# Performance work log

Hardware: AMD Instinct MI355X
Metric: run time of the kernel (lower is better)

The kernel has to match this reference:

```python
import jax, jax.numpy as jnp
import numpy as np


def _prelu(x, a):
    return jnp.where(x >= 0, x, a * x)


def _conv1x1(x, w, b, a):
    # x: (B,C,H,W), w: (O,C), b: (O,), a: PReLU scalar (shared, torch default)
    y = jnp.einsum('bchw,oc->bohw', x, w) + b[None, :, None, None]
    return _prelu(y, a)


def setup_inputs() -> dict:
    key = jax.random.key(0)
    ks = jax.random.split(key, 7)
    B, C, H, W = 8, 128, 256, 256
    std = 1.0 / np.sqrt(C)
    x = jax.random.normal(ks[0], (B, C, H, W), dtype=jnp.float32)
    Wf = jax.random.normal(ks[1], (C, C), dtype=jnp.float32) * std
    bf = jax.random.normal(ks[2], (C,), dtype=jnp.float32) * std
    Wg = jax.random.normal(ks[3], (C, C), dtype=jnp.float32) * std
    bg = jax.random.normal(ks[4], (C,), dtype=jnp.float32) * std
    Wh = jax.random.normal(ks[5], (C, C), dtype=jnp.float32) * std
    bh = jax.random.normal(ks[6], (C,), dtype=jnp.float32) * std
    af = jnp.float32(0.25)
    ag = jnp.float32(0.25)
    ah = jnp.float32(0.25)
    return {"x": x, "Wf": Wf, "bf": bf, "af": af,
            "Wg": Wg, "bg": bg, "ag": ag,
            "Wh": Wh, "bh": bh, "ah": ah}


def reference(x, Wf, bf, af, Wg, bg, ag, Wh, bh, ah):
    # 1x1 conv projections + PReLU
    map_f = _conv1x1(x, Wf, bf, af)          # (B,C,H,W)
    map_g = _conv1x1(x, Wg, bg, ag)          # (B,C,H,W)
    map_h = _conv1x1(x, Wh, bh, ah)          # (B,C,H,W)
    # map_f.transpose(2,3) @ map_g -> (B,C,W,W), unscaled single-head attention
    atten = jnp.einsum('bchw,bchv->bcwv', map_f, map_g)  # (B,C,W,W)
    atten = jax.nn.softmax(atten, axis=-1)
    # map_h @ atten -> (B,C,H,W)
    out = jnp.einsum('bchw,bcwv->bchv', map_h, atten)
    return out + x
```

## Files before the change

kernel.cpp:

```cpp
#include <hip/hip_runtime.h>

typedef __bf16 bf16_t;
typedef __bf16 bf16x8 __attribute__((ext_vector_type(8)));
typedef __bf16 bf16x4 __attribute__((ext_vector_type(4)));
typedef float  f32x4  __attribute__((ext_vector_type(4)));

#define HW_ 65536
#define C_  128

__device__ __forceinline__ int swz(int r) { return ((r ^ (r >> 3)) & 7) << 4; }

#define LGKM0()  asm volatile("s_waitcnt lgkmcnt(0)" ::: "memory")
#define VMCNT0() asm volatile("s_waitcnt vmcnt(0)" ::: "memory")
__device__ __forceinline__ void BAR() {
  asm volatile("" ::: "memory");
  __builtin_amdgcn_s_barrier();
  asm volatile("" ::: "memory");
}

typedef __attribute__((address_space(1))) const unsigned int g_u32;
typedef __attribute__((address_space(3))) unsigned int l_u32;

__global__ void wprep_kernel(const float* __restrict__ Wf, const float* __restrict__ Wg,
                             const float* __restrict__ Wh, bf16_t* __restrict__ dst)
{
  int i = blockIdx.x * 256 + threadIdx.x;
  int o = i >> 7, c = i & 127;
  int boff = (o * 256 + c * 2) ^ swz(o);
  char* d = (char*)dst;
  *(bf16_t*)(d + boff)         = (bf16_t)Wf[i];
  *(bf16_t*)(d + 32768 + boff) = (bf16_t)Wg[i];
  *(bf16_t*)(d + 65536 + boff) = (bf16_t)Wh[i];
}

__device__ __forceinline__ void stage_w(char* lds, const bf16_t* __restrict__ Wimg,
                                        int wv, int t)
{
  #pragma unroll
  for (int rep = 0; rep < 8; ++rep) {
    const char* src = (const char*)Wimg + (rep * 256 + t) * 16;
    char* dst = lds + 32768 + (rep * 4 + wv) * 1024;
    __builtin_amdgcn_global_load_lds((g_u32*)src, (l_u32*)dst, 16, 0, 0);
  }
}

__device__ __forceinline__ void conv_mfma(const char* lds, f32x4 (&acc)[2][8],
                                          int wv, int lr, int lq)
{
  const f32x4 fz = {0.f, 0.f, 0.f, 0.f};
  #pragma unroll
  for (int mf = 0; mf < 2; ++mf)
    #pragma unroll
    for (int nf = 0; nf < 8; ++nf)
      acc[mf][nf] = fz;

  #pragma unroll
  for (int ks = 0; ks < 4; ++ks) {
    int kb = ks * 32 + lq * 8;
    bf16x8 a[2], bb[8];
    #pragma unroll
    for (int mf = 0; mf < 2; ++mf) {
      int m = wv * 32 + mf * 16 + lr;
      a[mf] = *(const bf16x8*)(lds + 32768 + ((m * 256 + kb * 2) ^ swz(m)));
    }
    #pragma unroll
    for (int nf = 0; nf < 8; ++nf) {
      int n = nf * 16 + lr;
      bb[nf] = *(const bf16x8*)(lds + ((n * 256 + kb * 2) ^ swz(n)));
    }
    #pragma unroll
    for (int mf = 0; mf < 2; ++mf)
      #pragma unroll
      for (int nf = 0; nf < 8; ++nf)
        acc[mf][nf] = __builtin_amdgcn_mfma_f32_16x16x32_bf16(a[mf], bb[nf], acc[mf][nf], 0, 0, 0);
  }
}

template<bool HBLK>
__device__ __forceinline__ void conv_epi(const f32x4 (&acc)[2][8],
                                         const float* __restrict__ bias, float alpha,
                                         bf16_t* __restrict__ dst, size_t pb,
                                         int wv, int lr, int lq, int s0)
{
  #pragma unroll
  for (int mf = 0; mf < 2; ++mf) {
    #pragma unroll
    for (int i = 0; i < 4; ++i) {
      int o = wv * 32 + mf * 16 + lq * 4 + i;
      float bo = bias[o];
      #pragma unroll
      for (int nf = 0; nf < 8; ++nf) {
        int s = s0 + nf * 16 + lr;
        float v = acc[mf][nf][i] + bo;
        v = (v >= 0.f) ? v : alpha * v;
        size_t off;
        if (HBLK) {
          int h = s >> 8, w = s & 255;
          off = pb + (size_t)o * HW_ + (size_t)(w >> 6) * 16384 + h * 64 + (w & 63);
        } else {
          off = pb + (size_t)o * HW_ + s;
        }
        dst[off] = (bf16_t)v;
      }
    }
  }
}

__global__ __launch_bounds__(256, 2) void conv_kernel(
    const float* __restrict__ x, const bf16_t* __restrict__ Wimg,
    const float* __restrict__ bfp, const float* __restrict__ afp,
    const float* __restrict__ bgp, const float* __restrict__ agp,
    const float* __restrict__ bhp, const float* __restrict__ ahp,
    bf16_t* __restrict__ mF, bf16_t* __restrict__ mG, bf16_t* __restrict__ mH, int b0)
{
  __shared__ __align__(16) char lds[65536];
  const int t = threadIdx.x;
  const int bloc = blockIdx.y;
  const int s0 = blockIdx.x * 128;
  const size_t xbase = ((size_t)(b0 + bloc) * C_) * HW_ + s0;
  const int wv = t >> 6, lane = t & 63, lr = lane & 15, lq = lane >> 4;
  const size_t pb = (size_t)bloc * C_ * HW_;

  stage_w(lds, Wimg, wv, t);

  #pragma unroll
  for (int rep = 0; rep < 4; ++rep) {
    int q = rep * 256 + t;
    int c0 = (q >> 5) * 4, sl0 = (q & 31) * 4;
    f32x4 r[4];
    #pragma unroll
    for (int i = 0; i < 4; ++i)
      r[i] = *(const f32x4*)(x + xbase + (size_t)(c0 + i) * HW_ + sl0);
    #pragma unroll
    for (int js = 0; js < 4; ++js) {
      int s = sl0 + js;
      bf16x4 v;
      v[0] = (bf16_t)r[0][js]; v[1] = (bf16_t)r[1][js];
      v[2] = (bf16_t)r[2][js]; v[3] = (bf16_t)r[3][js];
      *(bf16x4*)(lds + ((s * 256 + c0 * 2) ^ swz(s))) = v;
    }
  }
  __syncthreads();

  f32x4 acc[2][8];

  conv_mfma(lds, acc, wv, lr, lq);
  BAR();
  stage_w(lds, Wimg + 16384, wv, t);
  conv_epi<false>(acc, bfp, afp[0], mF, pb, wv, lr, lq, s0);
  VMCNT0(); BAR();

  conv_mfma(lds, acc, wv, lr, lq);
  BAR();
  stage_w(lds, Wimg + 32768, wv, t);
  conv_epi<false>(acc, bgp, agp[0], mG, pb, wv, lr, lq, s0);
  VMCNT0(); BAR();

  conv_mfma(lds, acc, wv, lr, lq);
  conv_epi<true>(acc, bhp, ahp[0], mH, pb, wv, lr, lq, s0);
}

#define GT_OFF  32768
#define HS_OFF  131072
#define SMAX_OFF 151552
#define SSUM_OFF 153600
#define SMEM_BYTES 155648

__global__ __launch_bounds__(512, 2) void attn_kernel(
    const bf16_t* __restrict__ mF, const bf16_t* __restrict__ mG, const bf16_t* __restrict__ mH,
    const float* __restrict__ x, float* __restrict__ out, int b0)
{
  extern __shared__ __align__(16) char smem[];
  const int t = threadIdx.x;
  const int c = blockIdx.x, bloc = blockIdx.y;
  const int wv = t >> 6, lane = t & 63, lr = lane & 15, lq = lane >> 4;
  const int wr = wv >> 1, wc = wv & 1;
  const size_t plane  = ((size_t)bloc * C_ + c) * HW_;
  const size_t gplane = (((size_t)(b0 + bloc)) * C_ + c) * HW_;

  const f32x4 fz = {0.f, 0.f, 0.f, 0.f};
  f32x4 acc[4][8];
  #pragma unroll
  for (int mf = 0; mf < 4; ++mf)
    #pragma unroll
    for (int nf = 0; nf < 8; ++nf)
      acc[mf][nf] = fz;

  const int hq = t >> 5, wb8 = t & 31;

  bf16x8 pfF[4], pfG[4];
  #pragma unroll
  for (int i = 0; i < 4; ++i) {
    pfF[i] = *(const bf16x8*)(mF + plane + (size_t)(hq * 4 + i) * 256 + wb8 * 8);
    pfG[i] = *(const bf16x8*)(mG + plane + (size_t)(hq * 4 + i) * 256 + wb8 * 8);
  }

  for (int hb = 0; hb < 256; hb += 64) {
    BAR();
    #pragma unroll
    for (int j = 0; j < 8; ++j) {
      int w = wb8 * 8 + j;
      bf16x4 v; v[0] = pfF[0][j]; v[1] = pfF[1][j]; v[2] = pfF[2][j]; v[3] = pfF[3][j];
      *(bf16x4*)(smem + ((w * 128 + hq * 8) ^ swz(w))) = v;
      bf16x4 g; g[0] = pfG[0][j]; g[1] = pfG[1][j]; g[2] = pfG[2][j]; g[3] = pfG[3][j];
      *(bf16x4*)(smem + GT_OFF + ((w * 128 + hq * 8) ^ swz(w))) = g;
    }
    if (hb < 192) {
      #pragma unroll
      for (int i = 0; i < 4; ++i) {
        pfF[i] = *(const bf16x8*)(mF + plane + (size_t)(hb + 64 + hq * 4 + i) * 256 + wb8 * 8);
        pfG[i] = *(const bf16x8*)(mG + plane + (size_t)(hb + 64 + hq * 4 + i) * 256 + wb8 * 8);
      }
    }
    LGKM0(); BAR();
    #pragma unroll
    for (int k0 = 0; k0 < 64; k0 += 32) {
      int kb = k0 + lq * 8;
      bf16x8 a[4], bb[8];
      #pragma unroll
      for (int mf = 0; mf < 4; ++mf) {
        int m = wr * 64 + mf * 16 + lr;
        a[mf] = *(const bf16x8*)(smem + ((m * 128 + kb * 2) ^ swz(m)));
      }
      #pragma unroll
      for (int nf = 0; nf < 8; ++nf) {
        int n = wc * 128 + nf * 16 + lr;
        bb[nf] = *(const bf16x8*)(smem + GT_OFF + ((n * 128 + kb * 2) ^ swz(n)));
      }
      #pragma unroll
      for (int mf = 0; mf < 4; ++mf)
        #pragma unroll
        for (int nf = 0; nf < 8; ++nf)
          acc[mf][nf] = __builtin_amdgcn_mfma_f32_16x16x32_bf16(a[mf], bb[nf], acc[mf][nf], 0, 0, 0);
    }
  }

  float* smax = (float*)(smem + SMAX_OFF);
  float* ssum = (float*)(smem + SSUM_OFF);
  float rowm[4][4];
  #pragma unroll
  for (int mf = 0; mf < 4; ++mf)
    #pragma unroll
    for (int i = 0; i < 4; ++i) {
      float m = acc[mf][0][i];
      #pragma unroll
      for (int nf = 1; nf < 8; ++nf) m = fmaxf(m, acc[mf][nf][i]);
      #pragma unroll
      for (int d = 1; d < 16; d <<= 1) m = fmaxf(m, __shfl_xor(m, d));
      rowm[mf][i] = m;
    }
  if (lr == 0) {
    #pragma unroll
    for (int mf = 0; mf < 4; ++mf)
      #pragma unroll
      for (int i = 0; i < 4; ++i)
        smax[wc * 256 + wr * 64 + mf * 16 + lq * 4 + i] = rowm[mf][i];
  }
  __syncthreads();
  float m2[4][4], rs[4][4];
  #pragma unroll
  for (int mf = 0; mf < 4; ++mf)
    #pragma unroll
    for (int i = 0; i < 4; ++i) {
      int w = wr * 64 + mf * 16 + lq * 4 + i;
      m2[mf][i] = fmaxf(smax[w], smax[256 + w]);
      rs[mf][i] = 0.f;
    }
  #pragma unroll
  for (int mf = 0; mf < 4; ++mf)
    #pragma unroll
    for (int nf = 0; nf < 8; ++nf)
      #pragma unroll
      for (int i = 0; i < 4; ++i) {
        float e = __expf(acc[mf][nf][i] - m2[mf][i]);
        acc[mf][nf][i] = e;
        rs[mf][i] += e;
      }
  #pragma unroll
  for (int mf = 0; mf < 4; ++mf)
    #pragma unroll
    for (int i = 0; i < 4; ++i) {
      float s = rs[mf][i];
      #pragma unroll
      for (int d = 1; d < 16; d <<= 1) s += __shfl_xor(s, d);
      rs[mf][i] = s;
    }
  if (lr == 0) {
    #pragma unroll
    for (int mf = 0; mf < 4; ++mf)
      #pragma unroll
      for (int i = 0; i < 4; ++i)
        ssum[wc * 256 + wr * 64 + mf * 16 + lq * 4 + i] = rs[mf][i];
  }
  __syncthreads();
  #pragma unroll
  for (int mf = 0; mf < 4; ++mf)
    #pragma unroll
    for (int i = 0; i < 4; ++i) {
      int w = wr * 64 + mf * 16 + lq * 4 + i;
      float rinv = 1.f / (ssum[w] + ssum[256 + w]);
      #pragma unroll
      for (int nf = 0; nf < 8; ++nf) {
        int v_ = wc * 128 + nf * 16 + lr;
        *(bf16_t*)(smem + ((v_ * 512 + w * 2) ^ swz(v_))) = (bf16_t)(acc[mf][nf][i] * rinv);
      }
    }

  #pragma unroll
  for (int mf = 0; mf < 4; ++mf)
    #pragma unroll
    for (int nf = 0; nf < 8; ++nf)
      acc[mf][nf] = fz;

  bf16x8 hreg[2];
  {
    #pragma unroll
    for (int rep = 0; rep < 2; ++rep) {
      int u = rep * 512 + t;
      int h = u >> 2, wl0 = (u & 3) * 8;
      hreg[rep] = *(const bf16x8*)(mH + plane + h * 64 + wl0);
    }
  }

  for (int wk = 0; wk < 8; ++wk) {
    LGKM0(); BAR();
    {
      #pragma unroll
      for (int rep = 0; rep < 2; ++rep) {
        int u = rep * 512 + t;
        int h = u >> 2, wl0 = (u & 3) * 8;
        *(bf16x8*)(smem + HS_OFF + h * 80 + wl0 * 2) = hreg[rep];
      }
    }
    if (wk < 7) {
      const size_t hbase = plane + (size_t)((wk + 1) >> 1) * 16384 + (size_t)((wk + 1) & 1) * 32;
      #pragma unroll
      for (int rep = 0; rep < 2; ++rep) {
        int u = rep * 512 + t;
        int h = u >> 2, wl0 = (u & 3) * 8;
        hreg[rep] = *(const bf16x8*)(mH + hbase + h * 64 + wl0);
      }
    }
    LGKM0(); BAR();
    int kb = lq * 8;
    bf16x8 a[4], bb[8];
    #pragma unroll
    for (int mf = 0; mf < 4; ++mf) {
      int m = wr * 64 + mf * 16 + lr;
      a[mf] = *(const bf16x8*)(smem + HS_OFF + m * 80 + kb * 2);
    }
    #pragma unroll
    for (int nf = 0; nf < 8; ++nf) {
      int n = wc * 128 + nf * 16 + lr;
      int kg = wk * 32 + kb;
      bb[nf] = *(const bf16x8*)(smem + ((n * 512 + kg * 2) ^ swz(n)));
    }
    #pragma unroll
    for (int mf = 0; mf < 4; ++mf)
      #pragma unroll
      for (int nf = 0; nf < 8; ++nf)
        acc[mf][nf] = __builtin_amdgcn_mfma_f32_16x16x32_bf16(a[mf], bb[nf], acc[mf][nf], 0, 0, 0);
  }

  #pragma unroll
  for (int mf = 0; mf < 4; ++mf)
    #pragma unroll
    for (int i = 0; i < 4; ++i) {
      int h = wr * 64 + mf * 16 + lq * 4 + i;
      #pragma unroll
      for (int nf = 0; nf < 8; ++nf) {
        int v_ = wc * 128 + nf * 16 + lr;
        size_t off = gplane + (size_t)h * 256 + v_;
        out[off] = acc[mf][nf][i] + x[off];
      }
    }
}

extern "C" void kernel_launch(void* const* d_in, const int* in_sizes, int n_in,
                              void* d_out, int out_size, void* d_ws, size_t ws_size,
                              hipStream_t stream)
{
  (void)in_sizes; (void)n_in; (void)out_size;
  const float* x   = (const float*)d_in[0];
  const float* Wf  = (const float*)d_in[1];
  const float* bfp = (const float*)d_in[2];
  const float* afp = (const float*)d_in[3];
  const float* Wg  = (const float*)d_in[4];
  const float* bgp = (const float*)d_in[5];
  const float* agp = (const float*)d_in[6];
  const float* Wh  = (const float*)d_in[7];
  const float* bhp = (const float*)d_in[8];
  const float* ahp = (const float*)d_in[9];
  float* out = (float*)d_out;

  const size_t per_map_b = (size_t)C_ * HW_ * sizeof(bf16_t);
  int nb = 1;
  if      (ws_size >= 3 * 8 * per_map_b + 98304 * 2) nb = 8;
  else if (ws_size >= 3 * 4 * per_map_b + 98304 * 2) nb = 4;
  else if (ws_size >= 3 * 2 * per_map_b + 98304 * 2) nb = 2;

  hipFuncSetAttribute(reinterpret_cast<const void*>(attn_kernel),
                      hipFuncAttributeMaxDynamicSharedMemorySize, SMEM_BYTES);

  bf16_t* mF = (bf16_t*)d_ws;
  bf16_t* mG = mF + (size_t)nb * C_ * HW_;
  bf16_t* mH = mG + (size_t)nb * C_ * HW_;
  bf16_t* Wb = mH + (size_t)nb * C_ * HW_;

  wprep_kernel<<<dim3(64), 256, 0, stream>>>(Wf, Wg, Wh, Wb);

  for (int b0 = 0; b0 < 8; b0 += nb) {
    conv_kernel<<<dim3(512, nb), 256, 0, stream>>>(x, Wb, bfp, afp, bgp, agp,
                                                   bhp, ahp, mF, mG, mH, b0);
    attn_kernel<<<dim3(C_, nb), 512, SMEM_BYTES, stream>>>(mF, mG, mH, x, out, b0);
  }
}
```

Measured before the change: 389.6 us.

## Load map_h A-fragments directly from global with register prefetch, drop LDS staging

The conv epilogue now writes map_h in 32-wide column blocks so each attention-output k-chunk is a contiguous slab. The second GEMM loads H fragments straight from global into registers with a three-deep prefetch ring, instead of staging them through LDS with two barriers per k-step. Each wave now covers a 32x256 output strip rather than 64x128, and s_setprio is raised around the MFMA loop. This removes the H LDS region and the per-iteration barriers, but each wave now re-reads the full B tile from LDS and relies on global latency being hidden by the prefetch.

```diff
diff --git a/kernel.cpp b/kernel.cpp
--- a/kernel.cpp
+++ b/kernel.cpp
@@ -96,7 +96,7 @@
         size_t off;
         if (HBLK) {
           int h = s >> 8, w = s & 255;
-          off = pb + (size_t)o * HW_ + (size_t)(w >> 6) * 16384 + h * 64 + (w & 63);
+          off = pb + (size_t)o * HW_ + (size_t)(w >> 5) * 8192 + h * 32 + (w & 31);
         } else {
           off = pb + (size_t)o * HW_ + s;
         }
@@ -161,10 +161,9 @@
 }
 
 #define GT_OFF  32768
-#define HS_OFF  131072
-#define SMAX_OFF 151552
-#define SSUM_OFF 153600
-#define SMEM_BYTES 155648
+#define SMAX_OFF 131072
+#define SSUM_OFF 133120
+#define SMEM_BYTES 135168
 
 __global__ __launch_bounds__(512, 2) void attn_kernel(
     const bf16_t* __restrict__ mF, const bf16_t* __restrict__ mG, const bf16_t* __restrict__ mH,
@@ -306,72 +305,56 @@
       }
     }
 
-  #pragma unroll
-  for (int mf = 0; mf < 4; ++mf)
-    #pragma unroll
-    for (int nf = 0; nf < 8; ++nf)
-      acc[mf][nf] = fz;
-
-  bf16x8 hreg[2];
-  {
-    #pragma unroll
-    for (int rep = 0; rep < 2; ++rep) {
-      int u = rep * 512 + t;
-      int h = u >> 2, wl0 = (u & 3) * 8;
-      hreg[rep] = *(const bf16x8*)(mH + plane + h * 64 + wl0);
-    }
-  }
-
-  for (int wk = 0; wk < 8; ++wk) {
-    LGKM0(); BAR();
-    {
-      #pragma unroll
-      for (int rep = 0; rep < 2; ++rep) {
-        int u = rep * 512 + t;
-        int h = u >> 2, wl0 = (u & 3) * 8;
-        *(bf16x8*)(smem + HS_OFF + h * 80 + wl0 * 2) = hreg[rep];
-      }
-    }
-    if (wk < 7) {
-      const size_t hbase = plane + (size_t)((wk + 1) >> 1) * 16384 + (size_t)((wk + 1) & 1) * 32;
-      #pragma unroll
-      for (int rep = 0; rep < 2; ++rep) {
-        int u = rep * 512 + t;
-        int h = u >> 2, wl0 = (u & 3) * 8;
-        hreg[rep] = *(const bf16x8*)(mH + hbase + h * 64 + wl0);
-      }
-    }
-    LGKM0(); BAR();
-    int kb = lq * 8;
-    bf16x8 a[4], bb[8];
-    #pragma unroll
-    for (int mf = 0; mf < 4; ++mf) {
-      int m = wr * 64 + mf * 16 + lr;
-      a[mf] = *(const bf16x8*)(smem + HS_OFF + m * 80 + kb * 2);
-    }
-    #pragma unroll
-    for (int nf = 0; nf < 8; ++nf) {
-      int n = wc * 128 + nf * 16 + lr;
-      int kg = wk * 32 + kb;
-      bb[nf] = *(const bf16x8*)(smem + ((n * 512 + kg * 2) ^ swz(n)));
-    }
-    #pragma unroll
-    for (int mf = 0; mf < 4; ++mf)
-      #pragma unroll
-      for (int nf = 0; nf < 8; ++nf)
-        acc[mf][nf] = __builtin_amdgcn_mfma_f32_16x16x32_bf16(a[mf], bb[nf], acc[mf][nf], 0, 0, 0);
-  }
-
-  #pragma unroll
-  for (int mf = 0; mf < 4; ++mf)
-    #pragma unroll
-    for (int i = 0; i < 4; ++i) {
-      int h = wr * 64 + mf * 16 + lq * 4 + i;
-      #pragma unroll
-      for (int nf = 0; nf < 8; ++nf) {
-        int v_ = wc * 128 + nf * 16 + lr;
+  const bf16_t* hp = mH + plane;
+  bf16x8 aP[3][2];
+  #pragma unroll
+  for (int p = 0; p < 3; ++p)
+    #pragma unroll
+    for (int mf = 0; mf < 2; ++mf) {
+      int h = wv * 32 + mf * 16 + lr;
+      aP[p][mf] = *(const bf16x8*)(hp + (size_t)p * 8192 + h * 32 + lq * 8);
+    }
+
+  LGKM0(); BAR();
+
+  f32x4 oac[2][16];
+  #pragma unroll
+  for (int mf = 0; mf < 2; ++mf)
+    #pragma unroll
+    for (int nf = 0; nf < 16; ++nf)
+      oac[mf][nf] = fz;
+
+  __builtin_amdgcn_s_setprio(1);
+  #pragma unroll
+  for (int kc = 0; kc < 8; ++kc) {
+    bf16x8 a0 = aP[kc % 3][0], a1 = aP[kc % 3][1];
+    if (kc < 5) {
+      #pragma unroll
+      for (int mf = 0; mf < 2; ++mf) {
+        int h = wv * 32 + mf * 16 + lr;
+        aP[kc % 3][mf] = *(const bf16x8*)(hp + (size_t)(kc + 3) * 8192 + h * 32 + lq * 8);
+      }
+    }
+    #pragma unroll
+    for (int nf = 0; nf < 16; ++nf) {
+      int v_ = nf * 16 + lr;
+      bf16x8 bq = *(const bf16x8*)(smem + ((v_ * 512 + kc * 64 + lq * 16) ^ swz(v_)));
+      oac[0][nf] = __builtin_amdgcn_mfma_f32_16x16x32_bf16(a0, bq, oac[0][nf], 0, 0, 0);
+      oac[1][nf] = __builtin_amdgcn_mfma_f32_16x16x32_bf16(a1, bq, oac[1][nf], 0, 0, 0);
+    }
+  }
+  __builtin_amdgcn_s_setprio(0);
+
+  #pragma unroll
+  for (int mf = 0; mf < 2; ++mf)
+    #pragma unroll
+    for (int i = 0; i < 4; ++i) {
+      int h = wv * 32 + mf * 16 + lq * 4 + i;
+      #pragma unroll
+      for (int nf = 0; nf < 16; ++nf) {
+        int v_ = nf * 16 + lr;
         size_t off = gplane + (size_t)h * 256 + v_;
-        out[off] = acc[mf][nf][i] + x[off];
+        out[off] = oac[mf][nf][i] + x[off];
       }
     }
 }
```

Result: no change. 394.6 us (+1.3%).
